# Kernel tuning notes

Hardware: AMD Instinct MI355X
Metric: run time of the kernel (lower is better)

Reference implementation:

```python
import jax, jax.numpy as jnp
import numpy as np

B, T, D, U = 32, 2048, 512, 512


def setup_inputs() -> dict:
    key = jax.random.key(0)
    ks = jax.random.split(key, 6)
    scale = 0.05
    return {
        "values": jax.random.normal(ks[0], (B, T, D), dtype=jnp.float32),
        "query": jax.random.normal(ks[1], (B, D), dtype=jnp.float32),
        "W1_w": jax.random.normal(ks[2], (D, U), dtype=jnp.float32) * scale,
        "W1_b": jnp.zeros((U,), dtype=jnp.float32),
        "W2_w": jax.random.normal(ks[3], (D, U), dtype=jnp.float32) * scale,
        "W2_b": jnp.zeros((U,), dtype=jnp.float32),
        "V_w": jax.random.normal(ks[4], (U, 1), dtype=jnp.float32) * scale,
        "V_b": jnp.zeros((1,), dtype=jnp.float32),
    }


def reference(values, query, W1_w, W1_b, W2_w, W2_b, V_w, V_b):
    # values: [B, T, D]; query: [B, D]
    proj_v = jnp.einsum("btd,du->btu", values, W1_w) + W1_b          # [B, T, U]
    proj_q = (query @ W2_w + W2_b)[:, None, :]                        # [B, 1, U]
    score = jnp.tanh(proj_v + proj_q) @ V_w + V_b                     # [B, T, 1]
    attention_weights = jax.nn.softmax(score, axis=1)                 # [B, T, 1]
    context_vector = jnp.sum(attention_weights * values, axis=1)      # [B, D]
    return context_vector, attention_weights
```

## Files before the change

### kernel.cpp

```cpp
#include <hip/hip_runtime.h>
#include <hip/hip_bf16.h>
#include <stdint.h>


#define B_DIM 32
#define T_DIM 2048
#define D_DIM 512
#define U_DIM 512
#define M_DIM (B_DIM * T_DIM)

typedef short bf16x8 __attribute__((ext_vector_type(8)));
typedef float f32x4 __attribute__((ext_vector_type(4)));

__device__ __forceinline__ float fast_tanh(float x) {
    float e = __expf(2.0f * x);
    return 1.0f - __fdividef(2.0f, e + 1.0f);
}

__device__ __forceinline__ short bf16r(float x) {
    unsigned u = __float_as_uint(x);
    u += 0x7fffu + ((u >> 16) & 1u);
    return (short)(u >> 16);
}

__device__ __forceinline__ bf16x8 pack8v(f32x4 a, f32x4 b) {
    union { __hip_bfloat162 h[4]; bf16x8 v; } u;
    u.h[0] = __float22bfloat162_rn(make_float2(a[0], a[1]));
    u.h[1] = __float22bfloat162_rn(make_float2(a[2], a[3]));
    u.h[2] = __float22bfloat162_rn(make_float2(b[0], b[1]));
    u.h[3] = __float22bfloat162_rn(make_float2(b[2], b[3]));
    return u.v;
}


__global__ void prep_kernel(const float* __restrict__ W1_w,
                            const float* __restrict__ W1_b,
                            const float* __restrict__ W2_w,
                            const float* __restrict__ W2_b,
                            const float* __restrict__ query,
                            unsigned short* __restrict__ W1T,
                            float* __restrict__ qb) {
    __shared__ float red[256];
    const int tid = threadIdx.x;
    if (blockIdx.x < 128) {
        int n = blockIdx.x * 256 + tid;
        int uu    = n & 255;
        int kc    = (n >> 8) & 3;
        int kstep = (n >> 10) & 15;
        int ut    = n >> 14;
        int u  = ut * 256 + uu;
        int k0 = kstep * 32 + kc * 8;
        bf16x8 pk;
#pragma unroll
        for (int j = 0; j < 8; ++j)
            pk[j] = bf16r(W1_w[(size_t)(k0 + j) * U_DIM + u]);
        ((bf16x8*)W1T)[n] = pk;
    } else {
        int bid = blockIdx.x - 128;
        int b  = bid >> 3;
        int ug = bid & 7;
        int u  = ug * 64 + (tid & 63);
        int dq = tid >> 6;
        const float* q  = query + b * D_DIM + dq * 128;
        const float* w2 = W2_w + (size_t)(dq * 128) * U_DIM + u;
        float acc = 0.f;
#pragma unroll 8
        for (int d = 0; d < 128; ++d)
            acc += q[d] * w2[(size_t)d * U_DIM];
        red[tid] = acc;
        __syncthreads();
        if (tid < 64) {
            qb[b * U_DIM + u] = red[tid] + red[tid + 64] + red[tid + 128]
                              + red[tid + 192] + W2_b[u] + W1_b[u];
        }
    }
}

__global__ __launch_bounds__(256, 4) void score_kernel(
        const float* __restrict__ values,
        const unsigned short* __restrict__ W1T,
        const float* __restrict__ qb,
        const float* __restrict__ Vw,
        float* __restrict__ sP) {
    const int tid  = threadIdx.x;
    const int lane = tid & 63;
    const int w    = tid >> 6;
    const int l15  = lane & 15;
    const int quad = lane >> 4;
    const int wr   = w >> 1;
    const int wc   = w & 1;
    const int ut   = blockIdx.x & 1;
    const int mb   = (blockIdx.x >> 1) * 64;
    const int b    = mb >> 11;

    const float* arow0 = values + (size_t)(mb + wr * 32 + l15) * D_DIM + quad * 8;
    const float* arow1 = arow0 + 16 * D_DIM;
    const unsigned short* bbase =
        W1T + ((size_t)ut * 16384 + quad * 256 + wc * 128 + l15) * 8;

    f32x4 acc[2][8] = {};

#pragma unroll 1
    for (int ks = 0; ks < 16; ++ks) {
        const unsigned short* bks = bbase + (size_t)ks * 8192;
        bf16x8 bfr[8];
#pragma unroll
        for (int ui = 0; ui < 8; ++ui)
            bfr[ui] = *(const bf16x8*)(bks + (size_t)ui * 128);

        f32x4 a00 = *(const f32x4*)(arow0 + ks * 32);
        f32x4 a01 = *(const f32x4*)(arow0 + ks * 32 + 4);
        f32x4 a10 = *(const f32x4*)(arow1 + ks * 32);
        f32x4 a11 = *(const f32x4*)(arow1 + ks * 32 + 4);

        bf16x8 a0 = pack8v(a00, a01);
        bf16x8 a1 = pack8v(a10, a11);
        __builtin_amdgcn_s_setprio(1);
#pragma unroll
        for (int ui = 0; ui < 8; ++ui) {
            acc[0][ui] = __builtin_amdgcn_mfma_f32_16x16x32_bf16(a0, bfr[ui], acc[0][ui], 0, 0, 0);
            acc[1][ui] = __builtin_amdgcn_mfma_f32_16x16x32_bf16(a1, bfr[ui], acc[1][ui], 0, 0, 0);
        }
        __builtin_amdgcn_s_setprio(0);
    }

    const int ub = ut * 256 + wc * 128 + l15;
    float sm[2][4] = {};
#pragma unroll
    for (int ui = 0; ui < 8; ++ui) {
        const int u = ub + ui * 16;
        const float qv = qb[b * U_DIM + u];
        const float vw = Vw[u];
#pragma unroll
        for (int mt = 0; mt < 2; ++mt)
#pragma unroll
            for (int r = 0; r < 4; ++r)
                sm[mt][r] += fast_tanh(acc[mt][ui][r] + qv) * vw;
    }
#pragma unroll
    for (int mt = 0; mt < 2; ++mt)
#pragma unroll
        for (int r = 0; r < 4; ++r) {
            float v = sm[mt][r];
            v += __shfl_xor(v, 1, 64);
            v += __shfl_xor(v, 2, 64);
            v += __shfl_xor(v, 4, 64);
            v += __shfl_xor(v, 8, 64);
            sm[mt][r] = v;
        }
    if (l15 == 0) {
        const int slice = ut * 2 + wc;
#pragma unroll
        for (int mt = 0; mt < 2; ++mt)
#pragma unroll
            for (int r = 0; r < 4; ++r)
                sP[(size_t)slice * M_DIM + mb + wr * 32 + mt * 16 + quad * 4 + r] = sm[mt][r];
    }
}

__global__ void softmax_kernel(const float* __restrict__ sP,
                               float* __restrict__ out) {
    const int b = blockIdx.x;
    const int tid = threadIdx.x;

    float v[8];
    float mx = -1e30f;
#pragma unroll
    for (int i = 0; i < 8; ++i) {
        int m = b * T_DIM + i * 256 + tid;
        v[i] = sP[m] + sP[M_DIM + m] + sP[2 * M_DIM + m] + sP[3 * M_DIM + m];
        mx = fmaxf(mx, v[i]);
    }
#pragma unroll
    for (int off = 1; off < 64; off <<= 1)
        mx = fmaxf(mx, __shfl_xor(mx, off, 64));
    __shared__ float redm[4];
    if ((tid & 63) == 0) redm[tid >> 6] = mx;
    __syncthreads();
    mx = fmaxf(fmaxf(redm[0], redm[1]), fmaxf(redm[2], redm[3]));

    float sum = 0.f;
#pragma unroll
    for (int i = 0; i < 8; ++i) {
        v[i] = __expf(v[i] - mx);
        sum += v[i];
    }
#pragma unroll
    for (int off = 1; off < 64; off <<= 1)
        sum += __shfl_xor(sum, off, 64);
    __shared__ float reds[4];
    if ((tid & 63) == 0) reds[tid >> 6] = sum;
    __syncthreads();
    sum = reds[0] + reds[1] + reds[2] + reds[3];

    const float inv = 1.0f / sum;
#pragma unroll
    for (int i = 0; i < 8; ++i)
        out[B_DIM * D_DIM + b * T_DIM + i * 256 + tid] = v[i] * inv;
}

__global__ void context_kernel(const float* __restrict__ values,
                               const float* __restrict__ weights,
                               float* __restrict__ P) {
    __shared__ float sw[64];
    __shared__ float red[512];
    const int tc = blockIdx.x;
    const int b  = blockIdx.y;
    const int tid = threadIdx.x;
    const int d4 = tid & 127;
    const int th = tid >> 7;

    if (tid < 64) sw[tid] = weights[b * T_DIM + tc * 64 + tid];
    __syncthreads();

    const float4* vb = (const float4*)(values + ((size_t)b * T_DIM + tc * 64) * D_DIM) + d4;
    float4 acc = {0.f, 0.f, 0.f, 0.f};
#pragma unroll 8
    for (int i = th; i < 64; i += 2) {
        float wv = sw[i];
        float4 vv = vb[(size_t)i * 128];
        acc.x += wv * vv.x; acc.y += wv * vv.y;
        acc.z += wv * vv.z; acc.w += wv * vv.w;
    }
    if (th == 1) ((float4*)red)[d4] = acc;
    __syncthreads();
    if (th == 0) {
        float4 o = ((float4*)red)[d4];
        acc.x += o.x; acc.y += o.y; acc.z += o.z; acc.w += o.w;
        *(float4*)(P + ((size_t)(b * 32 + tc)) * 512 + d4 * 4) = acc;
    }
}

__global__ void reduce_kernel(const float* __restrict__ P,
                              float* __restrict__ ctx) {
    const int g = blockIdx.x * 256 + threadIdx.x;
    const int b = g >> 9, d = g & 511;
    float s = 0.f;
#pragma unroll
    for (int tc = 0; tc < 32; ++tc)
        s += P[((size_t)(b * 32 + tc)) * 512 + d];
    ctx[g] = s;
}

extern "C" void kernel_launch(void* const* d_in, const int* in_sizes, int n_in,
                              void* d_out, int out_size, void* d_ws, size_t ws_size,
                              hipStream_t stream) {
    const float* values = (const float*)d_in[0];
    const float* query  = (const float*)d_in[1];
    const float* W1_w   = (const float*)d_in[2];
    const float* W1_b   = (const float*)d_in[3];
    const float* W2_w   = (const float*)d_in[4];
    const float* W2_b   = (const float*)d_in[5];
    const float* V_w    = (const float*)d_in[6];

    float* out = (float*)d_out;

    unsigned char* ws = (unsigned char*)d_ws;
    unsigned short* W1T = (unsigned short*)(ws);
    float* qb = (float*)(ws + 524288);
    float* sP = (float*)(ws + 524288 + 65536);
    float* P  = (float*)(ws + 524288 + 65536 + 1048576);

    prep_kernel<<<384, 256, 0, stream>>>(W1_w, W1_b, W2_w, W2_b, query, W1T, qb);
    score_kernel<<<2048, 256, 0, stream>>>(values, W1T, qb, V_w, sP);
    softmax_kernel<<<B_DIM, 256, 0, stream>>>(sP, out);
    context_kernel<<<dim3(32, B_DIM), 256, 0, stream>>>(values, out + B_DIM * D_DIM, P);
    reduce_kernel<<<64, 256, 0, stream>>>(P, out);
}
```

Before: 303.8 us.

## Fuse score, softmax and context into one kernel with online-softmax combine

The score GEMM, the per-chunk softmax statistics and the weighted context sum now run in a single kernel. Each 512-thread block handles a 64-row chunk across all 512 U columns, so per-slice score partials are reduced in LDS instead of global memory. Each block writes a local max, sum and unnormalized context partial, and a small combine kernel rescales them flash-style to produce the final context and attention weights. This removes a second full pass over values and two kernel launches. In exchange, block size grows to 512 threads and grid size halves, which may lower occupancy for the MFMA loop.

```diff
diff --git a/kernel.cpp b/kernel.cpp
--- a/kernel.cpp
+++ b/kernel.cpp
@@ -76,27 +76,33 @@
     }
 }
 
-__global__ __launch_bounds__(256, 4) void score_kernel(
+__global__ __launch_bounds__(512, 4) void fused_kernel(
         const float* __restrict__ values,
         const unsigned short* __restrict__ W1T,
         const float* __restrict__ qb,
         const float* __restrict__ Vw,
-        float* __restrict__ sP) {
+        float* __restrict__ sP,
+        float* __restrict__ Pms,
+        float* __restrict__ Pctx) {
+    __shared__ float sred[4][64];
+    __shared__ float ew[64];
+    __shared__ __align__(16) float red[4][512];
+
     const int tid  = threadIdx.x;
     const int lane = tid & 63;
     const int w    = tid >> 6;
     const int l15  = lane & 15;
     const int quad = lane >> 4;
-    const int wr   = w >> 1;
-    const int wc   = w & 1;
-    const int ut   = blockIdx.x & 1;
-    const int mb   = (blockIdx.x >> 1) * 64;
+    const int wr   = w >> 2;
+    const int wc   = w & 3;
+    const int chunk = blockIdx.x;
+    const int mb   = chunk * 64;
     const int b    = mb >> 11;
 
     const float* arow0 = values + (size_t)(mb + wr * 32 + l15) * D_DIM + quad * 8;
     const float* arow1 = arow0 + 16 * D_DIM;
     const unsigned short* bbase =
-        W1T + ((size_t)ut * 16384 + quad * 256 + wc * 128 + l15) * 8;
+        W1T + ((size_t)(wc >> 1) * 16384 + quad * 256 + (wc & 1) * 128 + l15) * 8;
 
     f32x4 acc[2][8] = {};
 
@@ -124,7 +130,7 @@
         __builtin_amdgcn_s_setprio(0);
     }
 
-    const int ub = ut * 256 + wc * 128 + l15;
+    const int ub = wc * 128 + l15;
     float sm[2][4] = {};
 #pragma unroll
     for (int ui = 0; ui < 8; ++ui) {
@@ -149,97 +155,94 @@
             sm[mt][r] = v;
         }
     if (l15 == 0) {
-        const int slice = ut * 2 + wc;
 #pragma unroll
         for (int mt = 0; mt < 2; ++mt)
 #pragma unroll
             for (int r = 0; r < 4; ++r)
-                sP[(size_t)slice * M_DIM + mb + wr * 32 + mt * 16 + quad * 4 + r] = sm[mt][r];
-    }
-}
-
-__global__ void softmax_kernel(const float* __restrict__ sP,
+                sred[wc][wr * 32 + mt * 16 + quad * 4 + r] = sm[mt][r];
+    }
+    __syncthreads();
+
+    if (tid < 64) {
+        float s = sred[0][tid] + sred[1][tid] + sred[2][tid] + sred[3][tid];
+        sP[mb + tid] = s;
+        float m = s;
+#pragma unroll
+        for (int off = 1; off < 64; off <<= 1)
+            m = fmaxf(m, __shfl_xor(m, off, 64));
+        float e = __expf(s - m);
+        ew[tid] = e;
+        float S = e;
+#pragma unroll
+        for (int off = 1; off < 64; off <<= 1)
+            S += __shfl_xor(S, off, 64);
+        if (tid == 0) { Pms[chunk * 2] = m; Pms[chunk * 2 + 1] = S; }
+    }
+    __syncthreads();
+
+    {
+        const int d4 = tid & 127;
+        const int th = tid >> 7;
+        const float4* vb = (const float4*)(values + (size_t)(mb + th * 16) * D_DIM) + d4;
+        float4 a = {0.f, 0.f, 0.f, 0.f};
+#pragma unroll
+        for (int i = 0; i < 16; ++i) {
+            float e = ew[th * 16 + i];
+            float4 v = vb[(size_t)i * 128];
+            a.x += e * v.x; a.y += e * v.y;
+            a.z += e * v.z; a.w += e * v.w;
+        }
+        ((float4*)red)[th * 128 + d4] = a;
+    }
+    __syncthreads();
+    if (tid < 128) {
+        float4 o0 = ((float4*)red)[tid];
+        float4 o1 = ((float4*)red)[128 + tid];
+        float4 o2 = ((float4*)red)[256 + tid];
+        float4 o3 = ((float4*)red)[384 + tid];
+        float4 o;
+        o.x = o0.x + o1.x + o2.x + o3.x;
+        o.y = o0.y + o1.y + o2.y + o3.y;
+        o.z = o0.z + o1.z + o2.z + o3.z;
+        o.w = o0.w + o1.w + o2.w + o3.w;
+        *(float4*)(Pctx + (size_t)chunk * 512 + tid * 4) = o;
+    }
+}
+
+__global__ void combine_kernel(const float* __restrict__ Pctx,
+                               const float* __restrict__ Pms,
+                               const float* __restrict__ sP,
                                float* __restrict__ out) {
-    const int b = blockIdx.x;
+    __shared__ float sc[32];
+    const int b   = blockIdx.x;
     const int tid = threadIdx.x;
 
-    float v[8];
-    float mx = -1e30f;
-#pragma unroll
-    for (int i = 0; i < 8; ++i) {
-        int m = b * T_DIM + i * 256 + tid;
-        v[i] = sP[m] + sP[M_DIM + m] + sP[2 * M_DIM + m] + sP[3 * M_DIM + m];
-        mx = fmaxf(mx, v[i]);
-    }
-#pragma unroll
-    for (int off = 1; off < 64; off <<= 1)
-        mx = fmaxf(mx, __shfl_xor(mx, off, 64));
-    __shared__ float redm[4];
-    if ((tid & 63) == 0) redm[tid >> 6] = mx;
-    __syncthreads();
-    mx = fmaxf(fmaxf(redm[0], redm[1]), fmaxf(redm[2], redm[3]));
-
-    float sum = 0.f;
-#pragma unroll
-    for (int i = 0; i < 8; ++i) {
-        v[i] = __expf(v[i] - mx);
-        sum += v[i];
-    }
-#pragma unroll
-    for (int off = 1; off < 64; off <<= 1)
-        sum += __shfl_xor(sum, off, 64);
-    __shared__ float reds[4];
-    if ((tid & 63) == 0) reds[tid >> 6] = sum;
-    __syncthreads();
-    sum = reds[0] + reds[1] + reds[2] + reds[3];
-
-    const float inv = 1.0f / sum;
-#pragma unroll
-    for (int i = 0; i < 8; ++i)
-        out[B_DIM * D_DIM + b * T_DIM + i * 256 + tid] = v[i] * inv;
-}
-
-__global__ void context_kernel(const float* __restrict__ values,
-                               const float* __restrict__ weights,
-                               float* __restrict__ P) {
-    __shared__ float sw[64];
-    __shared__ float red[512];
-    const int tc = blockIdx.x;
-    const int b  = blockIdx.y;
-    const int tid = threadIdx.x;
-    const int d4 = tid & 127;
-    const int th = tid >> 7;
-
-    if (tid < 64) sw[tid] = weights[b * T_DIM + tc * 64 + tid];
-    __syncthreads();
-
-    const float4* vb = (const float4*)(values + ((size_t)b * T_DIM + tc * 64) * D_DIM) + d4;
-    float4 acc = {0.f, 0.f, 0.f, 0.f};
-#pragma unroll 8
-    for (int i = th; i < 64; i += 2) {
-        float wv = sw[i];
-        float4 vv = vb[(size_t)i * 128];
-        acc.x += wv * vv.x; acc.y += wv * vv.y;
-        acc.z += wv * vv.z; acc.w += wv * vv.w;
-    }
-    if (th == 1) ((float4*)red)[d4] = acc;
-    __syncthreads();
-    if (th == 0) {
-        float4 o = ((float4*)red)[d4];
-        acc.x += o.x; acc.y += o.y; acc.z += o.z; acc.w += o.w;
-        *(float4*)(P + ((size_t)(b * 32 + tc)) * 512 + d4 * 4) = acc;
-    }
-}
-
-__global__ void reduce_kernel(const float* __restrict__ P,
-                              float* __restrict__ ctx) {
-    const int g = blockIdx.x * 256 + threadIdx.x;
-    const int b = g >> 9, d = g & 511;
-    float s = 0.f;
-#pragma unroll
-    for (int tc = 0; tc < 32; ++tc)
-        s += P[((size_t)(b * 32 + tc)) * 512 + d];
-    ctx[g] = s;
+    float m = -1e30f;
+#pragma unroll
+    for (int c = 0; c < 32; ++c)
+        m = fmaxf(m, Pms[(b * 32 + c) * 2]);
+    if (tid < 32) sc[tid] = __expf(Pms[(b * 32 + tid) * 2] - m);
+    __syncthreads();
+    float S = 0.f;
+#pragma unroll
+    for (int c = 0; c < 32; ++c)
+        S += sc[c] * Pms[(b * 32 + c) * 2 + 1];
+    const float invS = 1.0f / S;
+
+#pragma unroll
+    for (int h = 0; h < 2; ++h) {
+        const int d = h * 256 + tid;
+        float a = 0.f;
+#pragma unroll
+        for (int c = 0; c < 32; ++c)
+            a += sc[c] * Pctx[(size_t)(b * 32 + c) * 512 + d];
+        out[b * D_DIM + d] = a * invS;
+    }
+#pragma unroll
+    for (int j = 0; j < 8; ++j) {
+        const int g = b * T_DIM + j * 256 + tid;
+        out[B_DIM * D_DIM + g] = __expf(sP[g] - m) * invS;
+    }
 }
 
 extern "C" void kernel_launch(void* const* d_in, const int* in_sizes, int n_in,
@@ -257,13 +260,12 @@
 
     unsigned char* ws = (unsigned char*)d_ws;
     unsigned short* W1T = (unsigned short*)(ws);
-    float* qb = (float*)(ws + 524288);
-    float* sP = (float*)(ws + 524288 + 65536);
-    float* P  = (float*)(ws + 524288 + 65536 + 1048576);
+    float* qb  = (float*)(ws + 524288);
+    float* sP  = (float*)(ws + 589824);
+    float* Pms = (float*)(ws + 851968);
+    float* Pctx= (float*)(ws + 860160);
 
     prep_kernel<<<384, 256, 0, stream>>>(W1_w, W1_b, W2_w, W2_b, query, W1T, qb);
-    score_kernel<<<2048, 256, 0, stream>>>(values, W1T, qb, V_w, sP);
-    softmax_kernel<<<B_DIM, 256, 0, stream>>>(sP, out);
-    context_kernel<<<dim3(32, B_DIM), 256, 0, stream>>>(values, out + B_DIM * D_DIM, P);
-    reduce_kernel<<<64, 256, 0, stream>>>(P, out);
-}
+    fused_kernel<<<1024, 512, 0, stream>>>(values, W1T, qb, V_w, sP, Pms, Pctx);
+    combine_kernel<<<B_DIM, 256, 0, stream>>>(Pctx, Pms, sP, out);
+}
```

Result: faster. 296.2 us (-2.5%).
